# Performance work log

Measured on AMD Instinct MI355X. Metric: run time of the kernel, lower is better.

Reference implementation:

```python
import jax, jax.numpy as jnp
import numpy as np

RELU_NEG_SLOPE = 0.2

def _gat_layer(x, W, a, src, dst, num_nodes, concat):
    # x: [N, Din]; W: [H, Din, F]; a: [H, 2F]; src/dst: [E]
    H, _, F = W.shape
    proj = jnp.einsum('nd,hdf->nhf', x, W)              # [N, H, F]
    a_self, a_nb = a[:, :F], a[:, F:]                   # [H, F] each
    alpha_self = jnp.einsum('nhf,hf->nh', proj, a_self) # [N, H]
    alpha_nb = jnp.einsum('nhf,hf->nh', proj, a_nb)     # [N, H]
    # edge score: a . [proj_dst || proj_src], dst = center node i, src = neighbor j
    e = jax.nn.leaky_relu(alpha_self[dst] + alpha_nb[src], RELU_NEG_SLOPE)  # [E, H]
    e_max = jax.ops.segment_max(e, dst, num_segments=num_nodes)
    e_exp = jnp.exp(e - e_max[dst])
    denom = jax.ops.segment_sum(e_exp, dst, num_segments=num_nodes)
    w = e_exp / denom[dst]                              # [E, H] softmax per dst node
    msg = proj[src] * w[:, :, None]                     # [E, H, F]
    out = jax.ops.segment_sum(msg, dst, num_segments=num_nodes)  # [N, H, F]
    if concat:
        return out.reshape(num_nodes, H * F)
    return out.mean(axis=1)


def setup_inputs() -> dict:
    key = jax.random.key(0)
    k1, k2, k3, k4, k5, k6 = jax.random.split(key, 6)
    N, Din, F1, H1 = 10000, 128, 64, 8
    Dmid = H1 * F1  # 512
    F2, H2 = 64, 1
    x = jax.random.normal(k1, (N, Din), dtype=jnp.float32)
    edges = jax.random.randint(k2, (2, 80000), 0, N, dtype=jnp.int64)
    W1 = jax.random.normal(k3, (H1, Din, F1), dtype=jnp.float32) / np.sqrt(Din)
    a1 = jax.random.normal(k4, (H1, 2 * F1), dtype=jnp.float32) / np.sqrt(2 * F1)
    W2 = jax.random.normal(k5, (H2, Dmid, F2), dtype=jnp.float32) / np.sqrt(Dmid)
    a2 = jax.random.normal(k6, (H2, 2 * F2), dtype=jnp.float32) / np.sqrt(2 * F2)
    return {"x": x, "edges": edges, "W1": W1, "a1": a1, "W2": W2, "a2": a2}


def reference(x, edges, W1, a1, W2, a2):
    N = x.shape[0]
    loops = jnp.arange(N, dtype=edges.dtype)
    # undirected graph + self loops (Graph.neighborhood adds both directions and self)
    src = jnp.concatenate([edges[0], edges[1], loops])
    dst = jnp.concatenate([edges[1], edges[0], loops])
    h = _gat_layer(x, W1, a1, src, dst, N, concat=True)   # [N, 512]
    h = jax.nn.elu(h)
    out = _gat_layer(h, W2, a2, src, dst, N, concat=False)  # [N, 64]
    return out
```

## Files before the change

### kernel.cpp

```cpp
#include <hip/hip_runtime.h>
#include <hip/hip_bf16.h>
#include <hip/hip_fp16.h>

#define RELU_NEG_SLOPE 0.2f

typedef _Float16 half8 __attribute__((ext_vector_type(8)));
typedef float f32x4 __attribute__((ext_vector_type(4)));

__device__ __forceinline__ float leaky(float e) {
    return (e > 0.f) ? e : RELU_NEG_SLOPE * e;
}

__device__ __forceinline__ float elu1(float x) {
    return (x > 0.f) ? x : (__expf(x) - 1.f);
}

__global__ __launch_bounds__(256) void stage_kernel(
    const float4* __restrict__ x4, const float* __restrict__ W1,
    const float* __restrict__ W2, float2* __restrict__ xh,
    __half* __restrict__ Bt1, __half* __restrict__ W2t,
    int* __restrict__ cnt, int n4, int t1, int t2, int N) {
    int i = blockIdx.x * 256 + threadIdx.x;
    if (i < n4) {
        float4 v = x4[i];
        float2 p;
        ((__half2*)&p)[0] = __floats2half2_rn(v.x, v.y);
        ((__half2*)&p)[1] = __floats2half2_rn(v.z, v.w);
        xh[i] = p;
    } else if (i < n4 + t1) {
        int j = i - n4;
        int f = j & 63;
        int d = (j >> 6) & 127;
        int h = j >> 13;
        Bt1[((h * 64 + f) << 7) + d] = __float2half(W1[j]);
    } else if (i < n4 + t1 + t2) {
        int j = i - n4 - t1;
        int f = j & 63;
        int d = j >> 6;
        W2t[f * 512 + d] = __float2half(W2[j]);
    } else if (i < n4 + t1 + t2 + N) {
        cnt[i - n4 - t1 - t2] = 0;
    }
}

__global__ __launch_bounds__(256) void scatter_ell(
    const int* __restrict__ edges, int E0, int* __restrict__ cnt,
    int* __restrict__ ell) {
    int i = blockIdx.x * 256 + threadIdx.x;
    if (i >= 2 * E0) return;
    int s = edges[i];
    int d = (i < E0) ? edges[E0 + i] : edges[i - E0];
    int pos = atomicAdd(&cnt[d], 1);
    ell[(d << 6) + pos] = s;
}

__global__ __launch_bounds__(256) void mfma_gemm1(
    const __half* __restrict__ Ah, const __half* __restrict__ Bt,
    const float* __restrict__ a1, __half* __restrict__ Cp,
    float* __restrict__ as_, float* __restrict__ an_, int M, int slabN) {
    const int lane = threadIdx.x & 63;
    const int wave = threadIdx.x >> 6;
    const int q = lane >> 4;
    const int l15 = lane & 15;
    const int h = blockIdx.x;
    const int mrow = blockIdx.y * 64 + wave * 16;

    f32x4 acc[4] = {{0.f, 0.f, 0.f, 0.f}, {0.f, 0.f, 0.f, 0.f},
                    {0.f, 0.f, 0.f, 0.f}, {0.f, 0.f, 0.f, 0.f}};
    const __half* Ap = Ah + (size_t)(mrow + l15) * 128 + q * 8;
    const __half* Bp = Bt + (size_t)(h * 64 + l15) * 128 + q * 8;
#pragma unroll
    for (int ks = 0; ks < 4; ks++) {
        half8 av = *(const half8*)(Ap + ks * 32);
#pragma unroll
        for (int t = 0; t < 4; t++) {
            half8 bv = *(const half8*)(Bp + (size_t)t * 16 * 128 + ks * 32);
            acc[t] = __builtin_amdgcn_mfma_f32_16x16x32_f16(av, bv, acc[t], 0, 0, 0);
        }
    }

    __half* Cs = Cp + (size_t)(h >> 1) * slabN + (h & 1) * 64;
    float asc[4], anc[4];
#pragma unroll
    for (int t = 0; t < 4; t++) {
        asc[t] = a1[h * 128 + t * 16 + l15];
        anc[t] = a1[h * 128 + 64 + t * 16 + l15];
    }
#pragma unroll
    for (int r = 0; r < 4; r++) {
        int mg = mrow + q * 4 + r;
        float ps = 0.f, pn = 0.f;
#pragma unroll
        for (int t = 0; t < 4; t++) {
            float v = acc[t][r];
            ps += v * asc[t];
            pn += v * anc[t];
            if (mg < M)
                Cs[(size_t)mg * 128 + t * 16 + l15] = __float2half(v);
        }
#pragma unroll
        for (int m = 8; m >= 1; m >>= 1) {
            ps += __shfl_xor(ps, m, 64);
            pn += __shfl_xor(pn, m, 64);
        }
        if (l15 == 0 && mg < M) {
            as_[mg * 8 + h] = ps;
            an_[mg * 8 + h] = pn;
        }
    }
}

__global__ __launch_bounds__(256) void agg_h8_sliced(
    const int* __restrict__ cnt, const int* __restrict__ ell,
    const __half* __restrict__ projp, const float* __restrict__ as_,
    const float* __restrict__ an_, __half* __restrict__ outh,
    int N, int slabN) {
    int bid = blockIdx.x;
    int hp = bid & 3;
    int rem = bid >> 2;
    int d = rem * 4 + (threadIdx.x >> 6);
    int lane = threadIdx.x & 63;
    if (d >= N) return;
    const int sub = lane >> 4;
    const int inner = lane & 15;
    const int hh = inner >> 3;
    const int h = hp * 2 + hh;
    const int c8 = (inner & 7) * 8;

    int deg = cnt[d];
    const int* row = ell + (d << 6);
    float asd = as_[d * 8 + h];
    const __half* slab = projp + (size_t)hp * slabN;

    float acc[8] = {0.f, 0.f, 0.f, 0.f, 0.f, 0.f, 0.f, 0.f};
    float den = 0.f;
    if (sub == 0) {
        float e = __expf(leaky(asd + an_[d * 8 + h]));
        half8 v = *(const half8*)(slab + (size_t)d * 128 + hh * 64 + c8);
        den = e;
#pragma unroll
        for (int i = 0; i < 8; i++) acc[i] = e * (float)v[i];
    }
    for (int j0 = 0; j0 < deg; j0 += 4) {
        int j = j0 + sub;
        int jc = (j < deg) ? j : (deg - 1);
        int s = row[jc];
        float e = __expf(leaky(asd + an_[s * 8 + h]));
        if (j >= deg) e = 0.f;
        half8 v = *(const half8*)(slab + (size_t)s * 128 + hh * 64 + c8);
        den += e;
#pragma unroll
        for (int i = 0; i < 8; i++) acc[i] += e * (float)v[i];
    }

#pragma unroll
    for (int off = 32; off >= 16; off >>= 1) {
#pragma unroll
        for (int i = 0; i < 8; i++) acc[i] += __shfl_down(acc[i], off, 64);
        den += __shfl_down(den, off, 64);
    }

    if (sub == 0) {
        float r = 1.f / den;
        half8 o;
#pragma unroll
        for (int i = 0; i < 8; i++) o[i] = (_Float16)elu1(acc[i] * r);
        *(half8*)(outh + (size_t)d * 512 + h * 64 + c8) = o;
    }
}

__global__ __launch_bounds__(256) void mfma_gemm2(
    const __half* __restrict__ Ah, const __half* __restrict__ Bt,
    const float* __restrict__ a2, __half* __restrict__ Ch,
    float* __restrict__ as_, float* __restrict__ an_, int M) {
    const int lane = threadIdx.x & 63;
    const int wave = threadIdx.x >> 6;
    const int q = lane >> 4;
    const int l15 = lane & 15;
    const int mrow = blockIdx.x * 64 + wave * 16;

    f32x4 acc[4] = {{0.f, 0.f, 0.f, 0.f}, {0.f, 0.f, 0.f, 0.f},
                    {0.f, 0.f, 0.f, 0.f}, {0.f, 0.f, 0.f, 0.f}};
    const __half* Ap = Ah + (size_t)(mrow + l15) * 512 + q * 8;
    const __half* Bp = Bt + (size_t)l15 * 512 + q * 8;
#pragma unroll
    for (int ks = 0; ks < 16; ks++) {
        half8 av = *(const half8*)(Ap + ks * 32);
#pragma unroll
        for (int t = 0; t < 4; t++) {
            half8 bv = *(const half8*)(Bp + (size_t)t * 16 * 512 + ks * 32);
            acc[t] = __builtin_amdgcn_mfma_f32_16x16x32_f16(av, bv, acc[t], 0, 0, 0);
        }
    }

    float asc[4], anc[4];
#pragma unroll
    for (int t = 0; t < 4; t++) {
        asc[t] = a2[t * 16 + l15];
        anc[t] = a2[64 + t * 16 + l15];
    }
#pragma unroll
    for (int r = 0; r < 4; r++) {
        int mg = mrow + q * 4 + r;
        float ps = 0.f, pn = 0.f;
#pragma unroll
        for (int t = 0; t < 4; t++) {
            float v = acc[t][r];
            ps += v * asc[t];
            pn += v * anc[t];
            if (mg < M)
                Ch[(size_t)mg * 64 + t * 16 + l15] = __float2half(v);
        }
#pragma unroll
        for (int m = 8; m >= 1; m >>= 1) {
            ps += __shfl_xor(ps, m, 64);
            pn += __shfl_xor(pn, m, 64);
        }
        if (l15 == 0 && mg < M) {
            as_[mg] = ps;
            an_[mg] = pn;
        }
    }
}

__global__ __launch_bounds__(256) void agg_node_h1(
    const int* __restrict__ cnt, const int* __restrict__ ell,
    const __half* __restrict__ projh, const float* __restrict__ as_,
    const float* __restrict__ an_, float* __restrict__ out, int N) {
    int d = blockIdx.x * 4 + (threadIdx.x >> 6);
    int lane = threadIdx.x & 63;
    if (d >= N) return;
    int sub = lane >> 4;
    int fl = lane & 15;
    int deg = cnt[d];
    const int* row = ell + (d << 6);
    float asd = as_[d];

    float4 acc = make_float4(0.f, 0.f, 0.f, 0.f);
    float den = 0.f;
    for (int j0 = 0; j0 < deg; j0 += 4) {
        int j = j0 + sub;
        int jc = (j < deg) ? j : (deg - 1);
        int s = row[jc];
        float e = __expf(leaky(asd + an_[s]));
        if (j >= deg) e = 0.f;
        float2 raw = *(const float2*)(projh + (size_t)s * 64 + fl * 4);
        float2 p01 = __half22float2(*(__half2*)&raw.x);
        float2 p23 = __half22float2(*(__half2*)&raw.y);
        den += e;
        acc.x += e * p01.x;
        acc.y += e * p01.y;
        acc.z += e * p23.x;
        acc.w += e * p23.y;
    }

#pragma unroll
    for (int off = 32; off >= 16; off >>= 1) {
        acc.x += __shfl_down(acc.x, off, 64);
        acc.y += __shfl_down(acc.y, off, 64);
        acc.z += __shfl_down(acc.z, off, 64);
        acc.w += __shfl_down(acc.w, off, 64);
        den += __shfl_down(den, off, 64);
    }

    if (sub == 0) {
        float e = __expf(leaky(asd + an_[d]));
        float2 raw = *(const float2*)(projh + (size_t)d * 64 + fl * 4);
        float2 p01 = __half22float2(*(__half2*)&raw.x);
        float2 p23 = __half22float2(*(__half2*)&raw.y);
        den += e;
        acc.x += e * p01.x;
        acc.y += e * p01.y;
        acc.z += e * p23.x;
        acc.w += e * p23.y;
        float rden = 1.f / den;
        float4 r;
        r.x = acc.x * rden;
        r.y = acc.y * rden;
        r.z = acc.z * rden;
        r.w = acc.w * rden;
        *(float4*)(out + (size_t)d * 64 + fl * 4) = r;
    }
}

extern "C" void kernel_launch(void* const* d_in, const int* in_sizes, int n_in,
                              void* d_out, int out_size, void* d_ws, size_t ws_size,
                              hipStream_t stream) {
    const float* x  = (const float*)d_in[0];
    const int* edges = (const int*)d_in[1];
    const float* W1 = (const float*)d_in[2];
    const float* a1 = (const float*)d_in[3];
    const float* W2 = (const float*)d_in[4];
    const float* a2 = (const float*)d_in[5];

    const int Din = 128, H1 = 8, F = 64, Dmid = 512;
    const int N = in_sizes[0] / Din;
    const int E0 = in_sizes[1] / 2;
    const int Mpad = (N + 63) & ~63;
    const int slabN = Mpad * 128;

    char* base = (char*)d_ws;
    size_t off = 0;
    auto take = [&](size_t bytes) {
        void* p = base + off;
        off = (off + bytes + 255) & ~(size_t)255;
        return p;
    };
    __half* x_h    = (__half*)take((size_t)Mpad * Din * 2);
    __half* proj1p = (__half*)take((size_t)4 * slabN * 2);
    __half* hbufh  = (__half*)take((size_t)Mpad * Dmid * 2);
    __half* proj2h = (__half*)take((size_t)N * F * 2);
    __half* Bt1    = (__half*)take((size_t)Dmid * Din * 2);
    __half* W2t    = (__half*)take((size_t)F * Dmid * 2);
    float* as1 = (float*)take((size_t)N * H1 * 4);
    float* an1 = (float*)take((size_t)N * H1 * 4);
    float* as2 = (float*)take((size_t)N * 4);
    float* an2 = (float*)take((size_t)N * 4);
    int* cnt = (int*)take((size_t)N * 4);
    int* ell = (int*)take((size_t)N * 64 * 4);

    int n4 = N * Din / 4;
    int t1 = H1 * Din * F, t2 = Dmid * F;
    int total = n4 + t1 + t2 + N;
    stage_kernel<<<(total + 255) / 256, 256, 0, stream>>>(
        (const float4*)x, W1, W2, (float2*)x_h, Bt1, W2t, cnt, n4, t1, t2, N);

    scatter_ell<<<(2 * E0 + 255) / 256, 256, 0, stream>>>(edges, E0, cnt, ell);

    dim3 g1(H1, (N + 63) / 64);
    mfma_gemm1<<<g1, 256, 0, stream>>>(x_h, Bt1, a1, proj1p, as1, an1, N, slabN);

    int nbp = (N + 3) / 4;
    agg_h8_sliced<<<4 * nbp, 256, 0, stream>>>(cnt, ell, proj1p, as1, an1,
                                               hbufh, N, slabN);

    mfma_gemm2<<<(N + 63) / 64, 256, 0, stream>>>(hbufh, W2t, a2, proj2h,
                                                  as2, an2, N);

    agg_node_h1<<<(N + 3) / 4, 256, 0, stream>>>(cnt, ell, proj2h,
                                                 as2, an2, (float*)d_out, N);
}
```

Before: 145.1 us.

## Fuse edge scatter into GEMM1 launch and widen per-lane aggregation slice

The edge scatter into the ELL table and the first MFMA GEMM, which are independent, now run as one launch with a block-index split. This removes a kernel launch and lets the two phases overlap on the GPU. The layer-1 aggregation now has each lane cover 16 features instead of 8, so each wave walks 8 neighbors per iteration instead of 4. That gives more memory-level parallelism per wave, at the cost of more registers and an extra shuffle-reduction step.

```diff
diff --git a/kernel.cpp b/kernel.cpp
--- a/kernel.cpp
+++ b/kernel.cpp
@@ -43,27 +43,29 @@
     }
 }
 
-__global__ __launch_bounds__(256) void scatter_ell(
+__global__ __launch_bounds__(256) void scatter_gemm1(
     const int* __restrict__ edges, int E0, int* __restrict__ cnt,
-    int* __restrict__ ell) {
-    int i = blockIdx.x * 256 + threadIdx.x;
-    if (i >= 2 * E0) return;
-    int s = edges[i];
-    int d = (i < E0) ? edges[E0 + i] : edges[i - E0];
-    int pos = atomicAdd(&cnt[d], 1);
-    ell[(d << 6) + pos] = s;
-}
-
-__global__ __launch_bounds__(256) void mfma_gemm1(
+    int* __restrict__ ell, int nscat,
     const __half* __restrict__ Ah, const __half* __restrict__ Bt,
     const float* __restrict__ a1, __half* __restrict__ Cp,
     float* __restrict__ as_, float* __restrict__ an_, int M, int slabN) {
+    if (blockIdx.x < nscat) {
+        int i = blockIdx.x * 256 + threadIdx.x;
+        if (i >= 2 * E0) return;
+        int s = edges[i];
+        int d = (i < E0) ? edges[E0 + i] : edges[i - E0];
+        int pos = atomicAdd(&cnt[d], 1);
+        ell[(d << 6) + pos] = s;
+        return;
+    }
+    int bid2 = blockIdx.x - nscat;
+    const int h = bid2 & 7;
+    const int by = bid2 >> 3;
     const int lane = threadIdx.x & 63;
     const int wave = threadIdx.x >> 6;
     const int q = lane >> 4;
     const int l15 = lane & 15;
-    const int h = blockIdx.x;
-    const int mrow = blockIdx.y * 64 + wave * 16;
+    const int mrow = by * 64 + wave * 16;
 
     f32x4 acc[4] = {{0.f, 0.f, 0.f, 0.f}, {0.f, 0.f, 0.f, 0.f},
                     {0.f, 0.f, 0.f, 0.f}, {0.f, 0.f, 0.f, 0.f}};
@@ -121,51 +123,68 @@
     int d = rem * 4 + (threadIdx.x >> 6);
     int lane = threadIdx.x & 63;
     if (d >= N) return;
-    const int sub = lane >> 4;
-    const int inner = lane & 15;
-    const int hh = inner >> 3;
+    const int sub = lane >> 3;
+    const int inner = lane & 7;
+    const int hh = inner >> 2;
     const int h = hp * 2 + hh;
-    const int c8 = (inner & 7) * 8;
+    const int c16 = (inner & 3) * 16;
 
     int deg = cnt[d];
     const int* row = ell + (d << 6);
     float asd = as_[d * 8 + h];
     const __half* slab = projp + (size_t)hp * slabN;
 
-    float acc[8] = {0.f, 0.f, 0.f, 0.f, 0.f, 0.f, 0.f, 0.f};
+    float acc[16];
+#pragma unroll
+    for (int i = 0; i < 16; i++) acc[i] = 0.f;
     float den = 0.f;
     if (sub == 0) {
         float e = __expf(leaky(asd + an_[d * 8 + h]));
-        half8 v = *(const half8*)(slab + (size_t)d * 128 + hh * 64 + c8);
+        const __half* p = slab + (size_t)d * 128 + hh * 64 + c16;
+        half8 v0 = *(const half8*)p;
+        half8 v1 = *(const half8*)(p + 8);
         den = e;
 #pragma unroll
-        for (int i = 0; i < 8; i++) acc[i] = e * (float)v[i];
-    }
-    for (int j0 = 0; j0 < deg; j0 += 4) {
+        for (int i = 0; i < 8; i++) {
+            acc[i] = e * (float)v0[i];
+            acc[8 + i] = e * (float)v1[i];
+        }
+    }
+    for (int j0 = 0; j0 < deg; j0 += 8) {
         int j = j0 + sub;
         int jc = (j < deg) ? j : (deg - 1);
         int s = row[jc];
         float e = __expf(leaky(asd + an_[s * 8 + h]));
         if (j >= deg) e = 0.f;
-        half8 v = *(const half8*)(slab + (size_t)s * 128 + hh * 64 + c8);
+        const __half* p = slab + (size_t)s * 128 + hh * 64 + c16;
+        half8 v0 = *(const half8*)p;
+        half8 v1 = *(const half8*)(p + 8);
         den += e;
 #pragma unroll
-        for (int i = 0; i < 8; i++) acc[i] += e * (float)v[i];
-    }
-
-#pragma unroll
-    for (int off = 32; off >= 16; off >>= 1) {
-#pragma unroll
-        for (int i = 0; i < 8; i++) acc[i] += __shfl_down(acc[i], off, 64);
+        for (int i = 0; i < 8; i++) {
+            acc[i] += e * (float)v0[i];
+            acc[8 + i] += e * (float)v1[i];
+        }
+    }
+
+#pragma unroll
+    for (int off = 32; off >= 8; off >>= 1) {
+#pragma unroll
+        for (int i = 0; i < 16; i++) acc[i] += __shfl_down(acc[i], off, 64);
         den += __shfl_down(den, off, 64);
     }
 
     if (sub == 0) {
         float r = 1.f / den;
-        half8 o;
-#pragma unroll
-        for (int i = 0; i < 8; i++) o[i] = (_Float16)elu1(acc[i] * r);
-        *(half8*)(outh + (size_t)d * 512 + h * 64 + c8) = o;
+        half8 o0, o1;
+#pragma unroll
+        for (int i = 0; i < 8; i++) {
+            o0[i] = (_Float16)elu1(acc[i] * r);
+            o1[i] = (_Float16)elu1(acc[8 + i] * r);
+        }
+        __half* op = outh + (size_t)d * 512 + h * 64 + c16;
+        *(half8*)op = o0;
+        *(half8*)(op + 8) = o1;
     }
 }
 
@@ -325,10 +344,11 @@
     stage_kernel<<<(total + 255) / 256, 256, 0, stream>>>(
         (const float4*)x, W1, W2, (float2*)x_h, Bt1, W2t, cnt, n4, t1, t2, N);
 
-    scatter_ell<<<(2 * E0 + 255) / 256, 256, 0, stream>>>(edges, E0, cnt, ell);
-
-    dim3 g1(H1, (N + 63) / 64);
-    mfma_gemm1<<<g1, 256, 0, stream>>>(x_h, Bt1, a1, proj1p, as1, an1, N, slabN);
+    int nscat = (2 * E0 + 255) / 256;
+    int ngemm = H1 * ((N + 63) / 64);
+    scatter_gemm1<<<nscat + ngemm, 256, 0, stream>>>(
+        edges, E0, cnt, ell, nscat,
+        x_h, Bt1, a1, proj1p, as1, an1, N, slabN);
 
     int nbp = (N + 3) / 4;
     agg_h8_sliced<<<4 * nbp, 256, 0, stream>>>(cnt, ell, proj1p, as1, an1,
```

Result: no change. 143.7 us (-0.9%).
